# Kernel tuning notes

Measured on AMD Instinct MI355X. Metric: run time of the kernel, lower is better.

The kernel has to match this reference:

```python
import jax, jax.numpy as jnp
import numpy as np

NEURON_CDECAY = 0.5
NEURON_VTH = 0.5
SPIKE_WIN = 0.5
THETA_r = 0.021
THETA_s = 0.132
THETA_u = 0.529
THETA_v = -0.172


@jax.custom_vjp
def spike_fn(v):
    return (v > NEURON_VTH).astype(v.dtype)

def _spike_fwd(v):
    return spike_fn(v), v

def _spike_bwd(v, g):
    # rectangular pseudo-gradient: pass grad where |v - vth| < window
    return (g * (jnp.abs(v - NEURON_VTH) < SPIKE_WIN).astype(g.dtype),)

spike_fn.defvjp(_spike_fwd, _spike_bwd)


def lif_step(x, W, b, state):
    """One LIF neuron update. state = (current, volt, u, spike)."""
    c, v, u, s = state
    c = c * NEURON_CDECAY + x @ W.T + b
    v = v * (1.0 - s) + THETA_r * s
    u = u + s * THETA_s
    dv = v * v - v - u + c
    du = THETA_v * v + THETA_u * u
    v = v + dv
    u = u + du
    s = spike_fn(v)
    return (c, v, u, s)


def setup_inputs() -> dict:
    key = jax.random.key(0)
    ks = jax.random.split(key, 8)
    B, IN, H0, H1, OUT, T = 1024, 2048, 1024, 1024, 512, 16
    def lin(k, fan_out, fan_in):
        k1, k2 = jax.random.split(k)
        bound = 1.0 / np.sqrt(fan_in)
        W = jax.random.uniform(k1, (fan_out, fan_in), jnp.float32, -bound, bound)
        b = jax.random.uniform(k2, (fan_out,), jnp.float32, -bound, bound)
        return W, b
    W0, b0 = lin(ks[0], H0, IN)
    W1, b1 = lin(ks[1], H1, H0)
    Wout, bout = lin(ks[2], OUT, H1)
    in_pop_spikes = jax.random.uniform(ks[3], (B, IN, T), jnp.float32)
    return {"in_pop_spikes": in_pop_spikes, "W0": W0, "b0": b0, "W1": W1,
            "b1": b1, "Wout": Wout, "bout": bout, "batch_size": B}


def reference(in_pop_spikes, W0, b0, W1, b1, Wout, bout, batch_size):
    B = batch_size
    T = in_pop_spikes.shape[2]
    dt = in_pop_spikes.dtype
    def zeros4(d):
        return tuple(jnp.zeros((B, d), dt) for _ in range(4))
    init = (zeros4(W0.shape[0]), zeros4(W1.shape[0]), zeros4(Wout.shape[0]),
            jnp.zeros((B, Wout.shape[0]), dt))
    xs = jnp.transpose(in_pop_spikes, (2, 0, 1))  # [T, B, in_pop]
    def step(carry, x):
        h0, h1, o, acc = carry
        h0 = lif_step(x, W0, b0, h0)
        h1 = lif_step(h0[3], W1, b1, h1)
        o = lif_step(h1[3], Wout, bout, o)
        return (h0, h1, o, acc + o[3]), None
    (_, _, _, acc), _ = jax.lax.scan(step, init, xs)
    return acc / T
```

## Files before the change

### kernel.cpp

```cpp
#include <hip/hip_runtime.h>
#include <stdint.h>

#pragma clang fp contract(off)

constexpr int B_ = 1024, IN_ = 2048, H0_ = 1024, H1_ = 1024, OUT_ = 512;
constexpr int TC = 4;
constexpr int NCHUNK = 4;
constexpr int PQ = 512;

static __device__ __forceinline__ float fencef(float x) {
  asm volatile("" : "+v"(x));
  return x;
}

__global__ void transpose_x4(const float* __restrict__ X, float* __restrict__ Xt, int t0) {
  int idx = blockIdx.x * 256 + threadIdx.x;
  int b = idx >> 11, i = idx & (IN_ - 1);
  float4 v = *(const float4*)(X + (size_t)idx * 16 + t0);
  Xt[(size_t)b * IN_ + i] = v.x;
  Xt[(size_t)(B_ + b) * IN_ + i] = v.y;
  Xt[(size_t)(2 * B_ + b) * IN_ + i] = v.z;
  Xt[(size_t)(3 * B_ + b) * IN_ + i] = v.w;
}

__global__ __launch_bounds__(128) void gemm_panel(
    const float* __restrict__ A, const float* __restrict__ Bw,
    float* __restrict__ ZP, size_t pstride, int Ntiles, int K, int N) {
  __shared__ float As[32][132];
  __shared__ float Bs[32][68];

  int bid = blockIdx.x, cpx = gridDim.x >> 3;
  int wg = (bid & 7) * cpx + (bid >> 3);
  int tpp = (gridDim.x / ((K + PQ - 1) / PQ));
  int p = wg / tpp, r = wg - p * tpp;
  int bm = r / Ntiles, bn = r - bm * Ntiles;

  int tid = threadIdx.x;
  int tx = tid & 7, ty = tid >> 3;
  int rb = tid >> 1, cb = (tid & 1) * 16;

  float acc[8][8] = {};
  const size_t rowA = (size_t)(bm * 128 + tid) * K + p * PQ;
  const size_t rowB = (size_t)(bn * 64 + rb) * K + p * PQ;

  for (int kk = 0; kk < PQ; kk += 32) {
    float4 av[8], bv[4];
#pragma unroll
    for (int q = 0; q < 8; ++q)
      av[q] = *(const float4*)(A + rowA + kk + q * 4);
#pragma unroll
    for (int q = 0; q < 4; ++q)
      bv[q] = *(const float4*)(Bw + rowB + kk + cb + q * 4);
    __syncthreads();
#pragma unroll
    for (int q = 0; q < 8; ++q) {
      As[q * 4 + 0][tid] = av[q].x;
      As[q * 4 + 1][tid] = av[q].y;
      As[q * 4 + 2][tid] = av[q].z;
      As[q * 4 + 3][tid] = av[q].w;
    }
#pragma unroll
    for (int q = 0; q < 4; ++q) {
      Bs[cb + q * 4 + 0][rb] = bv[q].x;
      Bs[cb + q * 4 + 1][rb] = bv[q].y;
      Bs[cb + q * 4 + 2][rb] = bv[q].z;
      Bs[cb + q * 4 + 3][rb] = bv[q].w;
    }
    __syncthreads();
#pragma unroll
    for (int k = 0; k < 32; ++k) {
      float ar[8], br[8];
#pragma unroll
      for (int i = 0; i < 8; ++i) ar[i] = As[k][ty * 8 + i];
#pragma unroll
      for (int j = 0; j < 8; ++j) br[j] = Bs[k][tx * 8 + j];
#pragma unroll
      for (int i = 0; i < 8; ++i)
#pragma unroll
        for (int j = 0; j < 8; ++j)
          acc[i][j] = __builtin_fmaf(ar[i], br[j], acc[i][j]);
    }
  }
  float* Cb = ZP + p * pstride + (size_t)(bm * 128 + ty * 8) * N + bn * 64 + tx * 8;
#pragma unroll
  for (int i = 0; i < 8; ++i)
#pragma unroll
    for (int j = 0; j < 8; ++j)
      Cb[(size_t)i * N + j] = acc[i][j];
}

template <int NP>
__global__ void lif_chunk(const float* __restrict__ ZP, size_t pstride,
                          const float* __restrict__ bias,
                          float* __restrict__ stC, float* __restrict__ stV,
                          float* __restrict__ stU, float* __restrict__ Sout,
                          float* __restrict__ accB, float* __restrict__ Out,
                          int ncol, int first, int last) {
  int gid = blockIdx.x * 256 + threadIdx.x;
  int n = gid & (ncol - 1);
  float bn = bias[n];
  float c, v, u, s, acc;
  if (first) {
    c = 0.f; v = 0.f; u = 0.f; s = 0.f; acc = 0.f;
  } else {
    c = stC[gid]; v = stV[gid]; u = stU[gid];
    s = (v > 0.5f) ? 1.0f : 0.0f;
    acc = accB ? accB[gid] : 0.f;
  }
  size_t strideT = (size_t)B_ * (size_t)ncol;
#pragma unroll
  for (int tt = 0; tt < TC; ++tt) {
    float z = 0.f;
#pragma unroll
    for (int p = 0; p < NP; ++p)
      z = fencef(z + ZP[(size_t)p * pstride + (size_t)tt * strideT + gid]);
    float t1 = fencef(c * 0.5f);
    float t2 = fencef(t1 + z);
    c = fencef(t2 + bn);
    float w1 = fencef(1.0f - s);
    float w2 = fencef(v * w1);
    float w3 = fencef(0.021f * s);
    float vv = fencef(w2 + w3);
    float w4 = fencef(s * 0.132f);
    float uu = fencef(u + w4);
    float q1 = fencef(vv * vv);
    float q2 = fencef(q1 - vv);
    float q3 = fencef(q2 - uu);
    float dv = fencef(q3 + c);
    float r1 = fencef(-0.172f * vv);
    float r2 = fencef(0.529f * uu);
    float du = fencef(r1 + r2);
    v = fencef(vv + dv);
    u = fencef(uu + du);
    s = (v > 0.5f) ? 1.0f : 0.0f;
    if (Sout) Sout[(size_t)tt * strideT + gid] = s;
    acc = fencef(acc + s);
  }
  stC[gid] = c; stV[gid] = v; stU[gid] = u;
  if (accB) accB[gid] = acc;
  if (Out && last) Out[gid] = acc * 0.0625f;
}

extern "C" void kernel_launch(void* const* d_in, const int* in_sizes, int n_in,
                              void* d_out, int out_size, void* d_ws, size_t ws_size,
                              hipStream_t stream) {
  const float* X  = (const float*)d_in[0];
  const float* W0 = (const float*)d_in[1];
  const float* b0 = (const float*)d_in[2];
  const float* W1 = (const float*)d_in[3];
  const float* b1 = (const float*)d_in[4];
  const float* W2 = (const float*)d_in[5];
  const float* b2 = (const float*)d_in[6];
  float* Out = (float*)d_out;
  char* ws = (char*)d_ws;
  constexpr size_t MB = 1024ull * 1024ull;
  float* Xt   = (float*)(ws);
  float* ZP   = (float*)(ws + 32 * MB);
  float* S0c  = (float*)(ws + 96 * MB);
  float* S1c  = (float*)(ws + 112 * MB);
  float* st0c = (float*)(ws + 128 * MB);
  float* st0v = (float*)(ws + 132 * MB);
  float* st0u = (float*)(ws + 136 * MB);
  float* st1c = (float*)(ws + 140 * MB);
  float* st1v = (float*)(ws + 144 * MB);
  float* st1u = (float*)(ws + 148 * MB);
  float* st2c = (float*)(ws + 152 * MB);
  float* st2v = (float*)(ws + 154 * MB);
  float* st2u = (float*)(ws + 156 * MB);
  float* accB = (float*)(ws + 158 * MB);

  const size_t psH = (size_t)(TC * B_) * H0_;
  const size_t psO = (size_t)(TC * B_) * OUT_;

  for (int ci = 0; ci < NCHUNK; ++ci) {
    int first = (ci == 0) ? 1 : 0;
    int last = (ci == NCHUNK - 1) ? 1 : 0;
    transpose_x4<<<(B_ * IN_) / 256, 256, 0, stream>>>(X, Xt, ci * TC);
    gemm_panel<<<4 * (TC * B_ / 128) * (H0_ / 64), 128, 0, stream>>>(
        Xt, W0, ZP, psH, H0_ / 64, IN_, H0_);
    lif_chunk<4><<<(B_ * H0_) / 256, 256, 0, stream>>>(
        ZP, psH, b0, st0c, st0v, st0u, S0c, nullptr, nullptr, H0_, first, 0);
    gemm_panel<<<2 * (TC * B_ / 128) * (H1_ / 64), 128, 0, stream>>>(
        S0c, W1, ZP, psH, H1_ / 64, H0_, H1_);
    lif_chunk<2><<<(B_ * H1_) / 256, 256, 0, stream>>>(
        ZP, psH, b1, st1c, st1v, st1u, S1c, nullptr, nullptr, H1_, first, 0);
    gemm_panel<<<2 * (TC * B_ / 128) * (OUT_ / 64), 128, 0, stream>>>(
        S1c, W2, ZP, psO, OUT_ / 64, H1_, OUT_);
    lif_chunk<2><<<(B_ * OUT_) / 256, 256, 0, stream>>>(
        ZP, psO, b2, st2c, st2v, st2u, nullptr, accB, Out, OUT_, first, last);
  }
}
```

Baseline: 1.916 ms.

## Double-buffer GEMM shared tiles and use 256 threads with 8x4 micro-tiles

The FP32 panel GEMM now keeps two shared-memory buffers, so the global loads for the next K-slice are issued before the current slice is computed. This cuts one barrier per iteration and hides global load latency. The block also grows from 128 to 256 threads, with each thread holding an 8x4 accumulator tile instead of 8x8. That lowers register pressure and raises wave occupancy, at the cost of more LDS reads per FMA and twice the LDS footprint.

```diff
diff --git a/kernel.cpp b/kernel.cpp
--- a/kernel.cpp
+++ b/kernel.cpp
@@ -23,11 +23,11 @@
   Xt[(size_t)(3 * B_ + b) * IN_ + i] = v.w;
 }
 
-__global__ __launch_bounds__(128) void gemm_panel(
+__global__ __launch_bounds__(256) void gemm_panel(
     const float* __restrict__ A, const float* __restrict__ Bw,
     float* __restrict__ ZP, size_t pstride, int Ntiles, int K, int N) {
-  __shared__ float As[32][132];
-  __shared__ float Bs[32][68];
+  __shared__ float As[2][32][132];
+  __shared__ float Bs[2][32][68];
 
   int bid = blockIdx.x, cpx = gridDim.x >> 3;
   int wg = (bid & 7) * cpx + (bid >> 3);
@@ -36,56 +36,80 @@
   int bm = r / Ntiles, bn = r - bm * Ntiles;
 
   int tid = threadIdx.x;
-  int tx = tid & 7, ty = tid >> 3;
-  int rb = tid >> 1, cb = (tid & 1) * 16;
-
-  float acc[8][8] = {};
-  const size_t rowA = (size_t)(bm * 128 + tid) * K + p * PQ;
+  int ra = tid >> 1, ca = (tid & 1) * 16;
+  int rb = tid >> 2, cb = (tid & 3) * 8;
+  int tx = tid & 15, ty = tid >> 4;
+
+  float acc[8][4] = {};
+  const size_t rowA = (size_t)(bm * 128 + ra) * K + p * PQ;
   const size_t rowB = (size_t)(bn * 64 + rb) * K + p * PQ;
 
-  for (int kk = 0; kk < PQ; kk += 32) {
-    float4 av[8], bv[4];
-#pragma unroll
-    for (int q = 0; q < 8; ++q)
-      av[q] = *(const float4*)(A + rowA + kk + q * 4);
-#pragma unroll
-    for (int q = 0; q < 4; ++q)
-      bv[q] = *(const float4*)(Bw + rowB + kk + cb + q * 4);
+  float4 a0, a1, a2, a3, b0, b1;
+
+#define LOADT(kk)                                           \
+  do {                                                      \
+    a0 = *(const float4*)(A + rowA + (kk) + ca);            \
+    a1 = *(const float4*)(A + rowA + (kk) + ca + 4);        \
+    a2 = *(const float4*)(A + rowA + (kk) + ca + 8);        \
+    a3 = *(const float4*)(A + rowA + (kk) + ca + 12);       \
+    b0 = *(const float4*)(Bw + rowB + (kk) + cb);           \
+    b1 = *(const float4*)(Bw + rowB + (kk) + cb + 4);       \
+  } while (0)
+
+#define WRITET(buf)                                                   \
+  do {                                                                \
+    As[buf][ca + 0][ra] = a0.x;  As[buf][ca + 1][ra] = a0.y;          \
+    As[buf][ca + 2][ra] = a0.z;  As[buf][ca + 3][ra] = a0.w;          \
+    As[buf][ca + 4][ra] = a1.x;  As[buf][ca + 5][ra] = a1.y;          \
+    As[buf][ca + 6][ra] = a1.z;  As[buf][ca + 7][ra] = a1.w;          \
+    As[buf][ca + 8][ra] = a2.x;  As[buf][ca + 9][ra] = a2.y;          \
+    As[buf][ca + 10][ra] = a2.z; As[buf][ca + 11][ra] = a2.w;         \
+    As[buf][ca + 12][ra] = a3.x; As[buf][ca + 13][ra] = a3.y;         \
+    As[buf][ca + 14][ra] = a3.z; As[buf][ca + 15][ra] = a3.w;         \
+    Bs[buf][cb + 0][rb] = b0.x;  Bs[buf][cb + 1][rb] = b0.y;          \
+    Bs[buf][cb + 2][rb] = b0.z;  Bs[buf][cb + 3][rb] = b0.w;          \
+    Bs[buf][cb + 4][rb] = b1.x;  Bs[buf][cb + 5][rb] = b1.y;          \
+    Bs[buf][cb + 6][rb] = b1.z;  Bs[buf][cb + 7][rb] = b1.w;          \
+  } while (0)
+
+#define COMPUTET(buf)                                                 \
+  do {                                                                \
+    _Pragma("unroll")                                                 \
+    for (int k = 0; k < 32; ++k) {                                    \
+      float ar[8], br[4];                                             \
+      _Pragma("unroll")                                               \
+      for (int i = 0; i < 8; ++i) ar[i] = As[buf][k][ty * 8 + i];     \
+      _Pragma("unroll")                                               \
+      for (int j = 0; j < 4; ++j) br[j] = Bs[buf][k][tx * 4 + j];     \
+      _Pragma("unroll")                                               \
+      for (int i = 0; i < 8; ++i)                                     \
+        _Pragma("unroll")                                             \
+        for (int j = 0; j < 4; ++j)                                   \
+          acc[i][j] = __builtin_fmaf(ar[i], br[j], acc[i][j]);        \
+    }                                                                 \
+  } while (0)
+
+  LOADT(0);
+  WRITET(0);
+  __syncthreads();
+  int t = 1;
+  for (int kk = 32; kk < PQ; kk += 32, ++t) {
+    LOADT(kk);
+    COMPUTET((t - 1) & 1);
+    WRITET(t & 1);
     __syncthreads();
-#pragma unroll
-    for (int q = 0; q < 8; ++q) {
-      As[q * 4 + 0][tid] = av[q].x;
-      As[q * 4 + 1][tid] = av[q].y;
-      As[q * 4 + 2][tid] = av[q].z;
-      As[q * 4 + 3][tid] = av[q].w;
-    }
-#pragma unroll
-    for (int q = 0; q < 4; ++q) {
-      Bs[cb + q * 4 + 0][rb] = bv[q].x;
-      Bs[cb + q * 4 + 1][rb] = bv[q].y;
-      Bs[cb + q * 4 + 2][rb] = bv[q].z;
-      Bs[cb + q * 4 + 3][rb] = bv[q].w;
-    }
-    __syncthreads();
-#pragma unroll
-    for (int k = 0; k < 32; ++k) {
-      float ar[8], br[8];
-#pragma unroll
-      for (int i = 0; i < 8; ++i) ar[i] = As[k][ty * 8 + i];
-#pragma unroll
-      for (int j = 0; j < 8; ++j) br[j] = Bs[k][tx * 8 + j];
-#pragma unroll
-      for (int i = 0; i < 8; ++i)
-#pragma unroll
-        for (int j = 0; j < 8; ++j)
-          acc[i][j] = __builtin_fmaf(ar[i], br[j], acc[i][j]);
-    }
-  }
-  float* Cb = ZP + p * pstride + (size_t)(bm * 128 + ty * 8) * N + bn * 64 + tx * 8;
+  }
+  COMPUTET((t - 1) & 1);
+
+#undef LOADT
+#undef WRITET
+#undef COMPUTET
+
+  float* Cb = ZP + p * pstride + (size_t)(bm * 128 + ty * 8) * N + bn * 64 + tx * 4;
 #pragma unroll
   for (int i = 0; i < 8; ++i)
 #pragma unroll
-    for (int j = 0; j < 8; ++j)
+    for (int j = 0; j < 4; ++j)
       Cb[(size_t)i * N + j] = acc[i][j];
 }
 
@@ -176,15 +200,15 @@
     int first = (ci == 0) ? 1 : 0;
     int last = (ci == NCHUNK - 1) ? 1 : 0;
     transpose_x4<<<(B_ * IN_) / 256, 256, 0, stream>>>(X, Xt, ci * TC);
-    gemm_panel<<<4 * (TC * B_ / 128) * (H0_ / 64), 128, 0, stream>>>(
+    gemm_panel<<<4 * (TC * B_ / 128) * (H0_ / 64), 256, 0, stream>>>(
         Xt, W0, ZP, psH, H0_ / 64, IN_, H0_);
     lif_chunk<4><<<(B_ * H0_) / 256, 256, 0, stream>>>(
         ZP, psH, b0, st0c, st0v, st0u, S0c, nullptr, nullptr, H0_, first, 0);
-    gemm_panel<<<2 * (TC * B_ / 128) * (H1_ / 64), 128, 0, stream>>>(
+    gemm_panel<<<2 * (TC * B_ / 128) * (H1_ / 64), 256, 0, stream>>>(
         S0c, W1, ZP, psH, H1_ / 64, H0_, H1_);
     lif_chunk<2><<<(B_ * H1_) / 256, 256, 0, stream>>>(
         ZP, psH, b1, st1c, st1v, st1u, S1c, nullptr, nullptr, H1_, first, 0);
-    gemm_panel<<<2 * (TC * B_ / 128) * (OUT_ / 64), 128, 0, stream>>>(
+    gemm_panel<<<2 * (TC * B_ / 128) * (OUT_ / 64), 256, 0, stream>>>(
         S1c, W2, ZP, psO, OUT_ / 64, H1_, OUT_);
     lif_chunk<2><<<(B_ * OUT_) / 256, 256, 0, stream>>>(
         ZP, psO, b2, st2c, st2v, st2u, nullptr, accB, Out, OUT_, first, last);
```

After: 1.773 ms (median of 2 runs). 1.08x faster.
